# Kernel optimization log

Measured on AMD Instinct MI355X. Metric: run time of the kernel, lower is better.

## Reference

```python
import jax, jax.numpy as jnp
import numpy as np

N_OUT = 4096
N_IN = 4096
TOKENS = 8192
BITWIDTH = 4
GROUP_SIZE = 128
ZERO = 2 ** (BITWIDTH - 1)  # symmetric GPTQ zero-point


def setup_inputs() -> dict:
    key = jax.random.key(0)
    kx, kq, ks = jax.random.split(key, 3)
    x = jax.random.normal(kx, (TOKENS, N_IN), dtype=jnp.float32)
    qweight = jax.random.randint(kq, (N_OUT, N_IN), 0, 2 ** BITWIDTH, dtype=jnp.int32)
    scales = jax.random.uniform(ks, (N_OUT, N_IN // GROUP_SIZE), dtype=jnp.float32) * 0.02 + 0.001
    return {"x": x, "qweight": qweight, "scales": scales}


def reference(x, qweight, scales):
    # Dequantize: W[o, i] = (q[o, i] - zero) * scales[o, i // group_size]
    q = qweight.astype(x.dtype) - jnp.asarray(ZERO, dtype=x.dtype)
    # reshape input dim into (n_groups, group_size) and broadcast group scales
    qg = q.reshape(N_OUT, N_IN // GROUP_SIZE, GROUP_SIZE)
    w = (qg * scales[:, :, None].astype(x.dtype)).reshape(N_OUT, N_IN)
    # out = x @ W^T  -> [tokens, n_out]
    return jnp.einsum('ti,oi->to', x, w)
```

## Files before the change

### kernel.cpp

```cpp
#include <hip/hip_runtime.h>
#include <hip/hip_bf16.h>
#include <stdint.h>

#define TOKENS_C 8192
#define NIN_C    4096
#define NOUT_C   4096
#define GROUP_C  128
#define QZERO_C  8

typedef __bf16 bf16_t;
typedef __bf16  bf16x8 __attribute__((ext_vector_type(8)));
typedef float   f32x4  __attribute__((ext_vector_type(4)));
typedef int     i32x4  __attribute__((ext_vector_type(4)));

#define GAS __attribute__((address_space(1)))
#define LAS __attribute__((address_space(3)))

__device__ __forceinline__ void gload16(const void* g, void* l) {
  __builtin_amdgcn_global_load_lds((const GAS void*)g, (LAS void*)l, 16, 0, 0);
}

__global__ __launch_bounds__(256) void dequant_w_kernel(
    const int* __restrict__ qw, const float* __restrict__ sc,
    bf16_t* __restrict__ wb)
{
  const int t = blockIdx.x * 256 + threadIdx.x;
  const int64_t base = (int64_t)t * 8;
  const int o = (int)(base >> 12);
  const int i = (int)(base & 4095);
  const float s = sc[(o << 5) | (i >> 7)];
  i32x4 q0 = *(const i32x4*)(qw + base);
  i32x4 q1 = *(const i32x4*)(qw + base + 4);
  bf16x8 r;
  r[0] = (bf16_t)((float)(q0[0] - QZERO_C) * s);
  r[1] = (bf16_t)((float)(q0[1] - QZERO_C) * s);
  r[2] = (bf16_t)((float)(q0[2] - QZERO_C) * s);
  r[3] = (bf16_t)((float)(q0[3] - QZERO_C) * s);
  r[4] = (bf16_t)((float)(q1[0] - QZERO_C) * s);
  r[5] = (bf16_t)((float)(q1[1] - QZERO_C) * s);
  r[6] = (bf16_t)((float)(q1[2] - QZERO_C) * s);
  r[7] = (bf16_t)((float)(q1[3] - QZERO_C) * s);
  *(bf16x8*)(wb + base) = r;
}

__global__ __launch_bounds__(256) void cvt_x_kernel(
    const float* __restrict__ x, bf16_t* __restrict__ xb)
{
  const int t = blockIdx.x * 256 + threadIdx.x;
  const int64_t base = (int64_t)t * 8;
  f32x4 a = *(const f32x4*)(x + base);
  f32x4 b = *(const f32x4*)(x + base + 4);
  bf16x8 r;
  r[0] = (bf16_t)a[0]; r[1] = (bf16_t)a[1]; r[2] = (bf16_t)a[2]; r[3] = (bf16_t)a[3];
  r[4] = (bf16_t)b[0]; r[5] = (bf16_t)b[1]; r[6] = (bf16_t)b[2]; r[7] = (bf16_t)b[3];
  *(bf16x8*)(xb + base) = r;
}

#define BM 256
#define BN 256
#define BK 64
#define NT (NIN_C / BK)

__global__ __launch_bounds__(512, 2) void gemm_bt_kernel(
    const bf16_t* __restrict__ A,
    const bf16_t* __restrict__ B,
    float* __restrict__ C)
{
  constexpr int K = NIN_C, N = NOUT_C;
  constexpr int K2 = K * 2;
  __shared__ char smem[131072];

  const int tid  = threadIdx.x;
  const int lane = tid & 63;
  const int wid  = tid >> 6;
  const int wm   = wid >> 2;
  const int wn   = wid & 3;
  const int bm   = blockIdx.x;
  const int bn   = blockIdx.y;

  const int cswz = (((lane & 7) ^ (lane >> 3)) << 4);
  const char* Ag = (const char*)A;
  const char* Bg = (const char*)B;
  int64_t aso[2][2], bso[2][2];
#pragma unroll
  for (int h = 0; h < 2; ++h)
#pragma unroll
    for (int l = 0; l < 2; ++l) {
      const int r = h * 128 + (wid * 2 + l) * 8 + (lane >> 3);
      aso[h][l] = (int64_t)(bm * BM + r) * K2 + cswz;
      bso[h][l] = (int64_t)(bn * BN + r) * K2 + cswz;
    }
  const int sdst = wid * 2048 + (lane << 4);

#define STG_A(tt, h) { char* d_ = smem + (((tt) & 1) << 15) + ((h) << 14) + sdst; \
    gload16(Ag + aso[h][0] + (int64_t)(tt) * 128, d_);                            \
    gload16(Ag + aso[h][1] + (int64_t)(tt) * 128, d_ + 1024); }
#define STG_B(tt, h) { char* d_ = smem + 65536 + (((tt) & 1) << 15) + ((h) << 14) + sdst; \
    gload16(Bg + bso[h][0] + (int64_t)(tt) * 128, d_);                            \
    gload16(Bg + bso[h][1] + (int64_t)(tt) * 128, d_ + 1024); }

  const int frow  = lane & 15;
  const int fcol0 = (((lane >> 4) ^ (lane & 7)) << 4);

#define RD_B(dst, BB, ks)                                                      \
  _Pragma("unroll")                                                            \
  for (int j = 0; j < 4; ++j)                                                  \
    dst[j] = *(const bf16x8*)((BB) + ((wn & 1) * 64 + j * 16 + frow) * 128 +   \
                              (fcol0 ^ ((ks) << 6)));
#define RD_A(AB, mh, ks)                                                       \
  _Pragma("unroll")                                                            \
  for (int i = 0; i < 4; ++i)                                                  \
    a[i] = *(const bf16x8*)((AB) + ((mh) * 64 + i * 16 + frow) * 128 +         \
                            (fcol0 ^ ((ks) << 6)));
#define MM(mh, bv)                                                             \
  __builtin_amdgcn_s_setprio(1);                                               \
  _Pragma("unroll")                                                            \
  for (int i = 0; i < 4; ++i)                                                  \
    _Pragma("unroll")                                                          \
    for (int j = 0; j < 4; ++j)                                                \
      acc[(mh) * 4 + i][j] = __builtin_amdgcn_mfma_f32_16x16x32_bf16(          \
          a[i], bv[j], acc[(mh) * 4 + i][j], 0, 0, 0);                         \
  __builtin_amdgcn_s_setprio(0);
#define BAR __builtin_amdgcn_s_barrier()
#define WAITV(n) asm volatile("s_waitcnt vmcnt(" #n ")" ::: "memory")
#define SBAR0 __builtin_amdgcn_sched_barrier(0)

  const char* Ad0 = smem + wm * 16384;
  const char* Ad1 = smem + 32768 + wm * 16384;
  const char* Bd0 = smem + 65536 + (wn >> 1) * 16384;
  const char* Bd1 = smem + 98304 + (wn >> 1) * 16384;

  f32x4 acc[8][4] = {};
  bf16x8 a[4], b0[4], b1[4];

  STG_A(0, 0); STG_A(0, 1);
  STG_B(0, 0); STG_B(0, 1);
  STG_B(1, 0); STG_B(1, 1);
  WAITV(4);
  BAR; SBAR0;

  for (int i = 0; i < NT / 2 - 1; ++i) {
    const int t0 = 2 * i;
    RD_B(b0, Bd0, 0); RD_A(Ad0, 0, 0); STG_A(t0 + 1, 0); BAR; MM(0, b0); BAR;
    RD_B(b1, Bd0, 1); RD_A(Ad0, 1, 0); STG_A(t0 + 1, 1); BAR; MM(1, b0); BAR;
    RD_A(Ad0, 0, 1); STG_B(t0 + 2, 0); BAR; MM(0, b1); BAR;
    RD_A(Ad0, 1, 1); STG_B(t0 + 2, 1); WAITV(4); BAR; SBAR0; MM(1, b1); BAR;
    RD_B(b0, Bd1, 0); RD_A(Ad1, 0, 0); STG_A(t0 + 2, 0); BAR; MM(0, b0); BAR;
    RD_B(b1, Bd1, 1); RD_A(Ad1, 1, 0); STG_A(t0 + 2, 1); BAR; MM(1, b0); BAR;
    RD_A(Ad1, 0, 1); STG_B(t0 + 3, 0); BAR; MM(0, b1); BAR;
    RD_A(Ad1, 1, 1); STG_B(t0 + 3, 1); WAITV(4); BAR; SBAR0; MM(1, b1); BAR;
  }

  {
    RD_B(b0, Bd0, 0); RD_A(Ad0, 0, 0); STG_A(NT - 1, 0); BAR; MM(0, b0); BAR;
    RD_B(b1, Bd0, 1); RD_A(Ad0, 1, 0); STG_A(NT - 1, 1); BAR; MM(1, b0); BAR;
    RD_A(Ad0, 0, 1); BAR; MM(0, b1); BAR;
    RD_A(Ad0, 1, 1); WAITV(0); BAR; SBAR0; MM(1, b1); BAR;
    RD_B(b0, Bd1, 0); RD_A(Ad1, 0, 0); BAR; MM(0, b0); BAR;
    RD_B(b1, Bd1, 1); RD_A(Ad1, 1, 0); BAR; MM(1, b0); BAR;
    RD_A(Ad1, 0, 1); BAR; MM(0, b1); BAR;
    RD_A(Ad1, 1, 1); MM(1, b1);
  }

  const int crow0 = bm * BM + wm * 128;
  const int ccol0 = bn * BN + wn * 64;
  const int r0 = (lane >> 4) << 2;
  const int cc = lane & 15;
#pragma unroll
  for (int fi = 0; fi < 8; ++fi)
#pragma unroll
    for (int j = 0; j < 4; ++j) {
      f32x4 v = acc[fi][j];
#pragma unroll
      for (int r = 0; r < 4; ++r)
        C[(int64_t)(crow0 + fi * 16 + r0 + r) * N + (ccol0 + j * 16 + cc)] = v[r];
    }
#undef STG_A
#undef STG_B
#undef RD_A
#undef RD_B
#undef MM
#undef BAR
#undef WAITV
#undef SBAR0
}

__global__ __launch_bounds__(256) void naive_kernel(
    const float* __restrict__ x, const int* __restrict__ qw,
    const float* __restrict__ sc, float* __restrict__ out)
{
  const int64_t idx = (int64_t)blockIdx.x * 256 + threadIdx.x;
  const int tok = (int)(idx >> 12);
  const int o   = (int)(idx & 4095);
  const float* xr = x + (int64_t)tok * NIN_C;
  const int* qr = qw + (int64_t)o * NIN_C;
  float acc = 0.f;
  for (int g = 0; g < NIN_C / GROUP_C; ++g) {
    float s = sc[(o << 5) | g];
    float ga = 0.f;
#pragma unroll 4
    for (int i = g * GROUP_C; i < (g + 1) * GROUP_C; ++i)
      ga += xr[i] * (float)(qr[i] - QZERO_C);
    acc += s * ga;
  }
  out[idx] = acc;
}

extern "C" void kernel_launch(void* const* d_in, const int* in_sizes, int n_in,
                              void* d_out, int out_size, void* d_ws, size_t ws_size,
                              hipStream_t stream) {
  const float* x  = (const float*)d_in[0];
  const int*   qw = (const int*)d_in[1];
  const float* sc = (const float*)d_in[2];
  float* out = (float*)d_out;

  const size_t xb_bytes = (size_t)TOKENS_C * NIN_C * sizeof(bf16_t);
  const size_t wb_bytes = (size_t)NOUT_C * NIN_C * sizeof(bf16_t);

  if (ws_size < xb_bytes + wb_bytes) {
    const int64_t total = (int64_t)TOKENS_C * NOUT_C;
    naive_kernel<<<(int)(total / 256), 256, 0, stream>>>(x, qw, sc, out);
    return;
  }

  bf16_t* xb = (bf16_t*)d_ws;
  bf16_t* wb = (bf16_t*)((char*)d_ws + xb_bytes);

  {
    const int64_t elems = (int64_t)TOKENS_C * NIN_C;
    cvt_x_kernel<<<(int)(elems / 8 / 256), 256, 0, stream>>>(x, xb);
  }
  {
    const int64_t elems = (int64_t)NOUT_C * NIN_C;
    dequant_w_kernel<<<(int)(elems / 8 / 256), 256, 0, stream>>>(qw, sc, wb);
  }
  {
    dim3 grid(TOKENS_C / BM, NOUT_C / BN);
    gemm_bt_kernel<<<grid, 512, 0, stream>>>(xb, wb, out);
  }
}
```

Before: 267.2 us.

## Double-buffer A fragments in registers to overlap LDS reads with MFMA

Splits the A-fragment registers into two ping-pong sets so the LDS read of the next A sub-tile is issued before the MFMA block that uses the previous one. The first fragments of each k-tile are prefetched ahead of the loop and at each half-tile boundary. The goal is to hide LDS read latency behind matrix instructions instead of stalling on it each phase. It costs more VGPRs under a launch bound of 2 blocks per CU, which could cause spills.

```diff
diff --git a/kernel.cpp b/kernel.cpp
--- a/kernel.cpp
+++ b/kernel.cpp
@@ -107,19 +107,19 @@
   for (int j = 0; j < 4; ++j)                                                  \
     dst[j] = *(const bf16x8*)((BB) + ((wn & 1) * 64 + j * 16 + frow) * 128 +   \
                               (fcol0 ^ ((ks) << 6)));
-#define RD_A(AB, mh, ks)                                                       \
+#define RD_A(dst, AB, mh, ks)                                                  \
   _Pragma("unroll")                                                            \
   for (int i = 0; i < 4; ++i)                                                  \
-    a[i] = *(const bf16x8*)((AB) + ((mh) * 64 + i * 16 + frow) * 128 +         \
-                            (fcol0 ^ ((ks) << 6)));
-#define MM(mh, bv)                                                             \
+    dst[i] = *(const bf16x8*)((AB) + ((mh) * 64 + i * 16 + frow) * 128 +       \
+                              (fcol0 ^ ((ks) << 6)));
+#define MM(mh, av, bv)                                                         \
   __builtin_amdgcn_s_setprio(1);                                               \
   _Pragma("unroll")                                                            \
   for (int i = 0; i < 4; ++i)                                                  \
     _Pragma("unroll")                                                          \
     for (int j = 0; j < 4; ++j)                                                \
       acc[(mh) * 4 + i][j] = __builtin_amdgcn_mfma_f32_16x16x32_bf16(          \
-          a[i], bv[j], acc[(mh) * 4 + i][j], 0, 0, 0);                         \
+          av[i], bv[j], acc[(mh) * 4 + i][j], 0, 0, 0);                        \
   __builtin_amdgcn_s_setprio(0);
 #define BAR __builtin_amdgcn_s_barrier()
 #define WAITV(n) asm volatile("s_waitcnt vmcnt(" #n ")" ::: "memory")
@@ -131,35 +131,40 @@
   const char* Bd1 = smem + 98304 + (wn >> 1) * 16384;
 
   f32x4 acc[8][4] = {};
-  bf16x8 a[4], b0[4], b1[4];
+  bf16x8 aX[4], aY[4], b0[4], b1[4];
 
   STG_A(0, 0); STG_A(0, 1);
   STG_B(0, 0); STG_B(0, 1);
   STG_B(1, 0); STG_B(1, 1);
   WAITV(4);
   BAR; SBAR0;
+  RD_A(aX, Ad0, 0, 0);
+  RD_B(b0, Bd0, 0);
 
   for (int i = 0; i < NT / 2 - 1; ++i) {
     const int t0 = 2 * i;
-    RD_B(b0, Bd0, 0); RD_A(Ad0, 0, 0); STG_A(t0 + 1, 0); BAR; MM(0, b0); BAR;
-    RD_B(b1, Bd0, 1); RD_A(Ad0, 1, 0); STG_A(t0 + 1, 1); BAR; MM(1, b0); BAR;
-    RD_A(Ad0, 0, 1); STG_B(t0 + 2, 0); BAR; MM(0, b1); BAR;
-    RD_A(Ad0, 1, 1); STG_B(t0 + 2, 1); WAITV(4); BAR; SBAR0; MM(1, b1); BAR;
-    RD_B(b0, Bd1, 0); RD_A(Ad1, 0, 0); STG_A(t0 + 2, 0); BAR; MM(0, b0); BAR;
-    RD_B(b1, Bd1, 1); RD_A(Ad1, 1, 0); STG_A(t0 + 2, 1); BAR; MM(1, b0); BAR;
-    RD_A(Ad1, 0, 1); STG_B(t0 + 3, 0); BAR; MM(0, b1); BAR;
-    RD_A(Ad1, 1, 1); STG_B(t0 + 3, 1); WAITV(4); BAR; SBAR0; MM(1, b1); BAR;
-  }
-
-  {
-    RD_B(b0, Bd0, 0); RD_A(Ad0, 0, 0); STG_A(NT - 1, 0); BAR; MM(0, b0); BAR;
-    RD_B(b1, Bd0, 1); RD_A(Ad0, 1, 0); STG_A(NT - 1, 1); BAR; MM(1, b0); BAR;
-    RD_A(Ad0, 0, 1); BAR; MM(0, b1); BAR;
-    RD_A(Ad0, 1, 1); WAITV(0); BAR; SBAR0; MM(1, b1); BAR;
-    RD_B(b0, Bd1, 0); RD_A(Ad1, 0, 0); BAR; MM(0, b0); BAR;
-    RD_B(b1, Bd1, 1); RD_A(Ad1, 1, 0); BAR; MM(1, b0); BAR;
-    RD_A(Ad1, 0, 1); BAR; MM(0, b1); BAR;
-    RD_A(Ad1, 1, 1); MM(1, b1);
+    RD_A(aY, Ad0, 1, 0); RD_B(b1, Bd0, 1); STG_A(t0 + 1, 0); BAR; MM(0, aX, b0); BAR;
+    RD_A(aX, Ad0, 0, 1); STG_A(t0 + 1, 1); BAR; MM(1, aY, b0); BAR;
+    RD_A(aY, Ad0, 1, 1); STG_B(t0 + 2, 0); BAR; MM(0, aX, b1); BAR;
+    STG_B(t0 + 2, 1); WAITV(4); BAR; SBAR0;
+    RD_A(aX, Ad1, 0, 0); RD_B(b0, Bd1, 0); MM(1, aY, b1); BAR;
+    RD_A(aY, Ad1, 1, 0); RD_B(b1, Bd1, 1); STG_A(t0 + 2, 0); BAR; MM(0, aX, b0); BAR;
+    RD_A(aX, Ad1, 0, 1); STG_A(t0 + 2, 1); BAR; MM(1, aY, b0); BAR;
+    RD_A(aY, Ad1, 1, 1); STG_B(t0 + 3, 0); BAR; MM(0, aX, b1); BAR;
+    STG_B(t0 + 3, 1); WAITV(4); BAR; SBAR0;
+    RD_A(aX, Ad0, 0, 0); RD_B(b0, Bd0, 0); MM(1, aY, b1); BAR;
+  }
+
+  {
+    RD_A(aY, Ad0, 1, 0); RD_B(b1, Bd0, 1); STG_A(NT - 1, 0); BAR; MM(0, aX, b0); BAR;
+    RD_A(aX, Ad0, 0, 1); STG_A(NT - 1, 1); BAR; MM(1, aY, b0); BAR;
+    RD_A(aY, Ad0, 1, 1); BAR; MM(0, aX, b1); BAR;
+    WAITV(0); BAR; SBAR0;
+    RD_A(aX, Ad1, 0, 0); RD_B(b0, Bd1, 0); MM(1, aY, b1); BAR;
+    RD_A(aY, Ad1, 1, 0); RD_B(b1, Bd1, 1); BAR; MM(0, aX, b0); BAR;
+    RD_A(aX, Ad1, 0, 1); BAR; MM(1, aY, b0); BAR;
+    RD_A(aY, Ad1, 1, 1); BAR; MM(0, aX, b1); BAR;
+    MM(1, aY, b1);
   }
 
   const int crow0 = bm * BM + wm * 128;
```

Measured after the change: 268.4 us. About the same (+0.4%).
